# Performance work log

Measured on AMD Instinct MI355X. Metric: run time of the kernel, lower is better.

The kernel has to match this reference:

```python
import jax, jax.numpy as jnp
import numpy as np
import math

N, E, D, G = 100000, 1000000, 64, 128


def setup_inputs() -> dict:
    key = jax.random.key(0)
    ks = jax.random.split(key, 16)
    nrm = lambda k, shape: jax.random.normal(k, shape, jnp.float32) * 0.05
    return {
        "noise_x": jax.random.normal(ks[0], (N, D), jnp.float32),
        "edge_index": jax.random.randint(ks[1], (2, E), 0, N),
        "t": jax.random.randint(ks[2], (1,), 0, 1000),
        "train_anm": jax.random.randint(ks[3], (1000,), 0, N),
        "train_norm": jax.random.randint(ks[4], (5000,), 0, N),
        # time MLP (torch Linear weights stored as [in, out])
        "time_w1": nrm(ks[5], (D, D)), "time_b1": jnp.zeros((D,), jnp.float32),
        "time_w2": nrm(ks[6], (D, D)), "time_b2": jnp.zeros((D,), jnp.float32),
        "label_emb": nrm(ks[7], (2, D)),
        # GCNConv weights: down (D->G, G->G//2), up (G//2->G, 2G->D)
        "w0": nrm(ks[8], (D, G)), "b0": jnp.zeros((G,), jnp.float32),
        "w1": nrm(ks[9], (G, G // 2)), "b1": jnp.zeros((G // 2,), jnp.float32),
        "w2": nrm(ks[10], (G // 2, G)), "b2": jnp.zeros((G,), jnp.float32),
        "w3": nrm(ks[11], (2 * G, D)), "b3": jnp.zeros((D,), jnp.float32),
    }


def silu(x):
    return x * jax.nn.sigmoid(x)


def timestep_embedding(t, dim):
    # standard DDPM sinusoidal embedding; t: [1] int -> [1, dim]
    half = dim // 2
    freqs = jnp.exp(jnp.arange(half, dtype=jnp.float32) * (-math.log(10000.0) / (half - 1)))
    args = t.astype(jnp.float32)[:, None] * freqs[None, :]
    return jnp.concatenate([jnp.sin(args), jnp.cos(args)], axis=1)


def gcn_conv(x, w, b, src, dst, dinv):
    # PyG GCNConv: x' = D^-1/2 (A+I) D^-1/2 (x W) + b
    x = x @ w
    norm = dinv[src] * dinv[dst]                       # [E]
    agg = jax.ops.segment_sum(x[src] * norm[:, None], dst, num_segments=x.shape[0])
    agg = agg + x * (dinv * dinv)[:, None]             # self-loop term
    return agg + b


def reference(noise_x, edge_index, t, train_anm, train_norm,
              time_w1, time_b1, time_w2, time_b2, label_emb,
              w0, b0, w1, b1, w2, b2, w3, b3):
    n, d = noise_x.shape
    src, dst = edge_index[0], edge_index[1]
    # symmetric GCN normalization with self loops: deg = in-degree + 1
    deg = jnp.zeros((n,), jnp.float32).at[dst].add(1.0) + 1.0
    dinv = jax.lax.rsqrt(deg)

    # time embedding MLP (nonlinearity == SiLU)
    temb = timestep_embedding(t, d)
    temb = silu(temb @ time_w1 + time_b1) @ time_w2 + time_b2
    x_t = noise_x + temb                               # broadcast [1,D] over nodes

    # class-conditional label embedding matrix (anm rows set first, then norm)
    lab = jnp.zeros((n, d), noise_x.dtype)
    lab = lab.at[train_anm].set(label_emb[1])
    lab = lab.at[train_norm].set(label_emb[0])
    x_t = x_t + lab

    h0 = silu(gcn_conv(x_t, w0, b0, src, dst, dinv))   # residual link
    h1 = silu(gcn_conv(h0, w1, b1, src, dst, dinv))
    h2 = silu(gcn_conv(h1, w2, b2, src, dst, dinv))
    out = gcn_conv(jnp.concatenate([h2, h0], axis=1), w3, b3, src, dst, dinv)
    return silu(out)
```

## Files before the change

### kernel.cpp

```cpp
#include <hip/hip_runtime.h>
#include <math.h>


typedef unsigned short ushortT;
typedef __attribute__((ext_vector_type(8))) short short8v;
typedef __attribute__((ext_vector_type(4))) float f32x4;

#define CSR_CAP 48

__device__ __forceinline__ ushortT f2bf(float f) {
    unsigned int u = __float_as_uint(f);
    u += 0x7FFFu + ((u >> 16) & 1u);
    return (ushortT)(u >> 16);
}
__device__ __forceinline__ float bf2f(ushortT u) {
    return __uint_as_float(((unsigned int)u) << 16);
}

__global__ __launch_bounds__(256) void prep_kernel(int* __restrict__ cnt,
                                                   int* __restrict__ flag,
                                                   int n, int nblkN, int csBlk,
                                                   int* __restrict__ cs,
                                                   const float* __restrict__ w0,
                                                   const float* __restrict__ w1,
                                                   const float* __restrict__ w2,
                                                   const float* __restrict__ w3,
                                                   ushortT* __restrict__ wdst,
                                                   const int* __restrict__ t,
                                                   const float* __restrict__ tw1,
                                                   const float* __restrict__ tb1,
                                                   const float* __restrict__ tw2,
                                                   const float* __restrict__ tb2,
                                                   float* __restrict__ temb,
                                                   ushortT* __restrict__ bufXT,
                                                   ushortT* __restrict__ xw1) {
    int bid = blockIdx.x;
    if (bid < nblkN) {
        int i = bid * 256 + threadIdx.x;
        if (i < n) { cnt[i] = 0; flag[i] = 0; }
        return;
    }
    if (bid < nblkN + csBlk) {
        size_t total = (size_t)n * CSR_CAP;
        size_t base = ((size_t)(bid - nblkN) * 256 + threadIdx.x) * 16;
        int4 sv = make_int4(n, n, n, n);
#pragma unroll
        for (int j = 0; j < 4; ++j) {
            size_t p = base + j * 4;
            if (p + 4 <= total) *(int4*)(cs + p) = sv;
            else for (size_t q = p; q < total; ++q) cs[q] = n;
        }
        return;
    }
    if (bid < nblkN + csBlk + 160) {
        int i = (bid - nblkN - csBlk) * 256 + threadIdx.x;
        if (i >= 40960) return;
        const float* src; int ST, M, base;
        if (i < 8192)       { src = w0; ST = 8; M = 128; base = 0; }
        else if (i < 16384) { src = w1; ST = 4; M = 64;  base = 8192; }
        else if (i < 24576) { src = w2; ST = 8; M = 128; base = 16384; }
        else                { src = w3; ST = 4; M = 64;  base = 24576; }
        int idx = i - base;
        int j = idx & 7;
        int lane = (idx >> 3) & 63;
        int rest = idx >> 9;
        int s = rest % ST;
        int kq = rest / ST;
        int k = kq * 32 + (lane >> 4) * 8 + j;
        int col = s * 16 + (lane & 15);
        wdst[i] = f2bf(src[(size_t)k * M + col]);
        return;
    }
    __shared__ float emb[64], hid[64];
    int j = threadIdx.x;
    if (j >= 64 && j < 96)  ((unsigned int*)(bufXT + (size_t)n * 64))[j - 64] = 0u;
    if (j >= 96 && j < 128) ((unsigned int*)(xw1 + (size_t)n * 64))[j - 96] = 0u;
    if (j < 64) {
        float tf = (float)t[0];
        int h = j & 31;
        float freq = expf((float)h * -0.29710775393976190f);
        float arg = tf * freq;
        emb[j] = (j < 32) ? sinf(arg) : cosf(arg);
    }
    __syncthreads();
    if (j < 64) {
        float a = tb1[j];
        for (int k = 0; k < 64; ++k) a = fmaf(emb[k], tw1[k * 64 + j], a);
        hid[j] = a / (1.0f + expf(-a));
    }
    __syncthreads();
    if (j < 64) {
        float o = tb2[j];
        for (int k = 0; k < 64; ++k) o = fmaf(hid[k], tw2[k * 64 + j], o);
        temb[j] = o;
    }
}

__global__ __launch_bounds__(256) void flags_kernel(const int* __restrict__ anm, int na,
                                                    const int* __restrict__ nrm, int nn,
                                                    int* __restrict__ flag) {
    int i = blockIdx.x * 256 + threadIdx.x;
    if (i < na) atomicMax(&flag[anm[i]], 1);
    if (i < nn) atomicMax(&flag[nrm[i]], 2);
}

__global__ __launch_bounds__(256) void dinv_kernel(const int* __restrict__ cnt,
                                                   float* __restrict__ dinv, int n) {
    int i = blockIdx.x * 256 + threadIdx.x;
    if (i < n) dinv[i] = rsqrtf((float)cnt[i] + 1.0f);
}

__global__ __launch_bounds__(256) void fill_csr_kernel(const int* __restrict__ ei,
                                                       int* __restrict__ cnt,
                                                       int* __restrict__ cs, int e, int bdiv) {
    int xcd = blockIdx.x & 7;
    int i = (blockIdx.x >> 3) * 256 + threadIdx.x;
    if (i >= e) return;
    int dst = __builtin_nontemporal_load(ei + e + i);
    if (dst / bdiv != xcd) return;
    int src = __builtin_nontemporal_load(ei + i);
    int p = atomicAdd(&cnt[dst], 1);
    if (p < CSR_CAP) cs[(size_t)dst * CSR_CAP + p] = src;
}

__global__ __launch_bounds__(256) void xt_kernel(const float* __restrict__ nx,
                                                 const float* __restrict__ temb,
                                                 const float* __restrict__ lemb,
                                                 const int* __restrict__ flag,
                                                 const float* __restrict__ dinv,
                                                 ushortT* __restrict__ xt, int n) {
    int t = blockIdx.x * 256 + threadIdx.x;
    int total = n * 16;
    if (t >= total) return;
    int row = t >> 4;
    int c4 = (t & 15) * 4;
    float4 v = *(const float4*)(nx + (size_t)row * 64 + c4);
    float4 tv = *(const float4*)(temb + c4);
    v.x += tv.x; v.y += tv.y; v.z += tv.z; v.w += tv.w;
    int f = flag[row];
    if (f) {
        const float* le = lemb + (f == 1 ? 64 : 0);
        float4 lv = *(const float4*)(le + c4);
        v.x += lv.x; v.y += lv.y; v.z += lv.z; v.w += lv.w;
    }
    float dv = dinv[row];
    v.x *= dv; v.y *= dv; v.z *= dv; v.w *= dv;
    unsigned int p0 = (unsigned int)f2bf(v.x) | ((unsigned int)f2bf(v.y) << 16);
    unsigned int p1 = (unsigned int)f2bf(v.z) | ((unsigned int)f2bf(v.w) << 16);
    *(uint2*)(xt + (size_t)row * 64 + c4) = make_uint2(p0, p1);
}

template <int KQT, int ST, bool BIAS_SILU, bool OUT_BF16, bool CAT, bool SCALE>
__global__ __launch_bounds__(256) void mfma_gemm_kernel(const ushortT* __restrict__ A1,
                                                        const ushortT* __restrict__ A2,
                                                        const ushortT* __restrict__ Wswz,
                                                        const float* __restrict__ bias,
                                                        const float* __restrict__ dinvp,
                                                        void* __restrict__ Yv, int n) {
    constexpr int M = ST * 16;
    constexpr int KA = (CAT ? (KQT / 2) : KQT) * 32;
    const int lane = threadIdx.x & 63;
    const int wid = threadIdx.x >> 6;
    const int row0 = blockIdx.x * 64 + wid * 16;
    const int arow = row0 + (lane & 15);
    const int kb = (lane >> 4) * 8;

    f32x4 acc[ST];
#pragma unroll
    for (int s = 0; s < ST; ++s) acc[s] = (f32x4){0.f, 0.f, 0.f, 0.f};

#pragma unroll
    for (int kq = 0; kq < KQT; ++kq) {
        const ushortT* Asrc = (CAT && kq >= KQT / 2) ? A2 : A1;
        const int kloc = (CAT && kq >= KQT / 2) ? (kq - KQT / 2) * 32 : kq * 32;
        short8v a = *(const short8v*)(Asrc + (size_t)arow * KA + kloc + kb);
        const ushortT* wp = Wswz + ((size_t)(kq * ST) * 64 + lane) * 8;
#pragma unroll
        for (int s = 0; s < ST; ++s) {
            short8v b = *(const short8v*)(wp + (size_t)s * 64 * 8);
            acc[s] = __builtin_amdgcn_mfma_f32_16x16x32_bf16(a, b, acc[s], 0, 0, 0);
        }
    }

    const int dcol = lane & 15;
    const int drow0 = row0 + (lane >> 4) * 4;
    float sc[4];
    if (SCALE) {
#pragma unroll
        for (int r = 0; r < 4; ++r) sc[r] = (drow0 + r < n) ? dinvp[drow0 + r] : 0.f;
    }
#pragma unroll
    for (int s = 0; s < ST; ++s) {
        float bv = BIAS_SILU ? bias[s * 16 + dcol] : 0.f;
#pragma unroll
        for (int r = 0; r < 4; ++r) {
            int row = drow0 + r;
            if (row >= n) continue;
            float v = acc[s][r];
            if (BIAS_SILU) { v += bv; v = v / (1.0f + expf(-v)); }
            if (SCALE) v *= sc[r];
            if (OUT_BF16) ((ushortT*)Yv)[(size_t)row * M + s * 16 + dcol] = f2bf(v);
            else          ((float*)Yv)[(size_t)row * M + s * 16 + dcol] = v;
        }
    }
}

template <bool BIAS_SILU, bool OUT_BF16, bool POST_SCALE>
__global__ __launch_bounds__(256) void agg64_kernel(const ushortT* __restrict__ xw,
                                                    const int* __restrict__ cnt,
                                                    const int* __restrict__ cs,
                                                    const float* __restrict__ dinv,
                                                    const float* __restrict__ bias,
                                                    void* __restrict__ yv, int n) {
    int pair = (int)(((size_t)blockIdx.x * 256 + threadIdx.x) >> 6);
    int lane = threadIdx.x & 63;
    int nA = pair * 2;
    int nB = nA + 1;
    if (nA >= n) return;
    bool hasB = (nB < n);
    const int* rA = cs + (size_t)nA * CSR_CAP;
    const int* rB = cs + (size_t)nB * CSR_CAP;

    int ia[16], ib[16];
#pragma unroll
    for (int j = 0; j < 16; ++j) ia[j] = rA[j];
#pragma unroll
    for (int j = 0; j < 16; ++j) ib[j] = hasB ? rB[j] : n;

    float va[16], vb[16];
#pragma unroll
    for (int j = 0; j < 16; ++j) va[j] = bf2f(xw[(size_t)ia[j] * 64 + lane]);
#pragma unroll
    for (int j = 0; j < 16; ++j) vb[j] = bf2f(xw[(size_t)ib[j] * 64 + lane]);

    float a0 = (va[0] + va[1]) + (va[2] + va[3]);
    float a1 = (va[4] + va[5]) + (va[6] + va[7]);
    float a2 = (va[8] + va[9]) + (va[10] + va[11]);
    float a3 = (va[12] + va[13]) + (va[14] + va[15]);
    float b0 = (vb[0] + vb[1]) + (vb[2] + vb[3]);
    float b1 = (vb[4] + vb[5]) + (vb[6] + vb[7]);
    float b2 = (vb[8] + vb[9]) + (vb[10] + vb[11]);
    float b3 = (vb[12] + vb[13]) + (vb[14] + vb[15]);

    int cA = cnt[nA]; if (cA > CSR_CAP) cA = CSR_CAP;
    int cB = hasB ? cnt[nB] : 0; if (cB > CSR_CAP) cB = CSR_CAP;
    for (int j = 16; j < cA; ++j) a0 += bf2f(xw[(size_t)rA[j] * 64 + lane]);
    for (int j = 16; j < cB; ++j) b0 += bf2f(xw[(size_t)rB[j] * 64 + lane]);

    {
        float di = dinv[nA];
        float acc = (a0 + a1) + (a2 + a3);
        acc += bf2f(xw[(size_t)nA * 64 + lane]);
        acc *= di;
        if (BIAS_SILU) {
            acc += bias[lane];
            acc = acc / (1.0f + expf(-acc));
        }
        if (POST_SCALE) acc *= di;
        if (OUT_BF16) ((ushortT*)yv)[(size_t)nA * 64 + lane] = f2bf(acc);
        else          ((float*)yv)[(size_t)nA * 64 + lane] = acc;
    }
    if (hasB) {
        float di = dinv[nB];
        float acc = (b0 + b1) + (b2 + b3);
        acc += bf2f(xw[(size_t)nB * 64 + lane]);
        acc *= di;
        if (BIAS_SILU) {
            acc += bias[lane];
            acc = acc / (1.0f + expf(-acc));
        }
        if (POST_SCALE) acc *= di;
        if (OUT_BF16) ((ushortT*)yv)[(size_t)nB * 64 + lane] = f2bf(acc);
        else          ((float*)yv)[(size_t)nB * 64 + lane] = acc;
    }
}

extern "C" void kernel_launch(void* const* d_in, const int* in_sizes, int n_in,
                              void* d_out, int out_size, void* d_ws, size_t ws_size,
                              hipStream_t stream) {
    const float* noise_x = (const float*)d_in[0];
    const int*   edge    = (const int*)d_in[1];
    const int*   tptr    = (const int*)d_in[2];
    const int*   anm     = (const int*)d_in[3];
    const int*   nrm     = (const int*)d_in[4];
    const float* tw1     = (const float*)d_in[5];
    const float* tb1     = (const float*)d_in[6];
    const float* tw2     = (const float*)d_in[7];
    const float* tb2     = (const float*)d_in[8];
    const float* lemb    = (const float*)d_in[9];
    const float* w0      = (const float*)d_in[10];
    const float* b0      = (const float*)d_in[11];
    const float* w1      = (const float*)d_in[12];
    const float* b1      = (const float*)d_in[13];
    const float* w2      = (const float*)d_in[14];
    const float* b2      = (const float*)d_in[15];
    const float* w3      = (const float*)d_in[16];
    const float* b3      = (const float*)d_in[17];

    const int N = in_sizes[0] / 64;
    const int E = in_sizes[1] / 2;
    const int na = in_sizes[3];
    const int nn = in_sizes[4];
    float* out = (float*)d_out;

    char* ws = (char*)d_ws;
    size_t o = 0;
    auto carve = [&](size_t bytes) -> char* {
        char* p = ws + o;
        o += (bytes + 255) & ~(size_t)255;
        return p;
    };
    int*     cnt      = (int*)carve((size_t)N * 4);
    int*     flag     = (int*)carve((size_t)N * 4);
    int*     cs       = (int*)carve((size_t)N * CSR_CAP * 4);
    float*   dinv     = (float*)carve((size_t)N * 4);
    float*   temb     = (float*)carve(256);
    ushortT* wswz     = (ushortT*)carve(40960 * 2);
    ushortT* bufXT    = (ushortT*)carve((size_t)(N + 1) * 64 * 2);
    ushortT* aggX     = (ushortT*)carve((size_t)N * 64 * 2);
    ushortT* h0       = (ushortT*)carve((size_t)N * 128 * 2);
    ushortT* xw1      = (ushortT*)carve((size_t)(N + 1) * 64 * 2);
    ushortT* aggH1    = (ushortT*)carve((size_t)N * 64 * 2);
    ushortT* h2       = (ushortT*)carve((size_t)N * 128 * 2);
    ushortT* h1s      = bufXT;
    ushortT* z3       = xw1;

    const int nblkN = (N + 255) / 256;
    const int nblkE = (E + 255) / 256;
    const int nmax = na > nn ? na : nn;
    const int aggBlk = (N + 7) / 8;
    const int gblk = (N + 63) / 64;
    const int bdiv = (N + 7) / 8;
    const int csBlk = (int)(((size_t)N * CSR_CAP + 4095) / 4096);

    prep_kernel<<<nblkN + csBlk + 161, 256, 0, stream>>>(cnt, flag, N, nblkN, csBlk, cs,
                                                         w0, w1, w2, w3, wswz,
                                                         tptr, tw1, tb1, tw2, tb2, temb,
                                                         bufXT, xw1);
    flags_kernel<<<(nmax + 255) / 256, 256, 0, stream>>>(anm, na, nrm, nn, flag);
    fill_csr_kernel<<<8 * nblkE, 256, 0, stream>>>(edge, cnt, cs, E, bdiv);
    dinv_kernel<<<nblkN, 256, 0, stream>>>(cnt, dinv, N);
    xt_kernel<<<((size_t)N * 16 + 255) / 256, 256, 0, stream>>>(noise_x, temb, lemb, flag, dinv, bufXT, N);

    agg64_kernel<false, true, false><<<aggBlk, 256, 0, stream>>>(bufXT, cnt, cs, dinv, nullptr, aggX, N);
    mfma_gemm_kernel<2, 8, true, true, false, false><<<gblk, 256, 0, stream>>>(aggX, nullptr, wswz, b0, nullptr, h0, N);
    mfma_gemm_kernel<4, 4, false, true, false, true><<<gblk, 256, 0, stream>>>(h0, nullptr, wswz + 8192, nullptr, dinv, xw1, N);
    agg64_kernel<true, true, true><<<aggBlk, 256, 0, stream>>>(xw1, cnt, cs, dinv, b1, h1s, N);
    agg64_kernel<false, true, false><<<aggBlk, 256, 0, stream>>>(h1s, cnt, cs, dinv, nullptr, aggH1, N);
    mfma_gemm_kernel<2, 8, true, true, false, false><<<gblk, 256, 0, stream>>>(aggH1, nullptr, wswz + 16384, b2, nullptr, h2, N);
    mfma_gemm_kernel<8, 4, false, true, true, true><<<gblk, 256, 0, stream>>>(h2, h0, wswz + 24576, nullptr, dinv, z3, N);
    agg64_kernel<true, false, false><<<aggBlk, 256, 0, stream>>>(z3, cnt, cs, dinv, b3, out, N);
}
```

Measured before the change: 292.3 us.

## Bin edges by destination partition before CSR fill; aggregate four nodes per wave

Replaces the 8x-redundant edge scan (each XCD-targeted block re-reading all edges and filtering) with a two-pass scheme. A binning kernel uses a shared-memory histogram to write (src,dst) pairs into eight destination-range buckets, and a second kernel fills the CSR from each bucket. This cuts repeated reads of the edge list but adds an intermediate pairs buffer write and read. Separately, the aggregation kernel now handles four nodes per wave instead of two, putting more independent gathers in flight at the cost of higher register pressure.

Result: slower. 535.1 us (+83.0%).

```diff
diff --git a/kernel.cpp b/kernel.cpp
--- a/kernel.cpp
+++ b/kernel.cpp
@@ -19,6 +19,7 @@
 
 __global__ __launch_bounds__(256) void prep_kernel(int* __restrict__ cnt,
                                                    int* __restrict__ flag,
+                                                   int* __restrict__ bcnt,
                                                    int n, int nblkN, int csBlk,
                                                    int* __restrict__ cs,
                                                    const float* __restrict__ w0,
@@ -38,6 +39,7 @@
     if (bid < nblkN) {
         int i = bid * 256 + threadIdx.x;
         if (i < n) { cnt[i] = 0; flag[i] = 0; }
+        if (bid == 0 && threadIdx.x < 8) bcnt[threadIdx.x] = 0;
         return;
     }
     if (bid < nblkN + csBlk) {
@@ -110,17 +112,69 @@
     if (i < n) dinv[i] = rsqrtf((float)cnt[i] + 1.0f);
 }
 
-__global__ __launch_bounds__(256) void fill_csr_kernel(const int* __restrict__ ei,
-                                                       int* __restrict__ cnt,
-                                                       int* __restrict__ cs, int e, int bdiv) {
-    int xcd = blockIdx.x & 7;
-    int i = (blockIdx.x >> 3) * 256 + threadIdx.x;
-    if (i >= e) return;
-    int dst = __builtin_nontemporal_load(ei + e + i);
-    if (dst / bdiv != xcd) return;
-    int src = __builtin_nontemporal_load(ei + i);
-    int p = atomicAdd(&cnt[dst], 1);
-    if (p < CSR_CAP) cs[(size_t)dst * CSR_CAP + p] = src;
+__global__ __launch_bounds__(256) void bin_kernel(const int* __restrict__ ei,
+                                                  int* __restrict__ bcnt,
+                                                  int2* __restrict__ pairs,
+                                                  int e, int bdiv, int capb) {
+    __shared__ int hist[8];
+    __shared__ int base[8];
+    __shared__ int cur[8];
+    int t = threadIdx.x;
+    if (t < 8) { hist[t] = 0; cur[t] = 0; }
+    __syncthreads();
+    int i0 = blockIdx.x * 2048 + t;
+    int bk[8], sr[8], ds[8];
+#pragma unroll
+    for (int j = 0; j < 8; ++j) {
+        int i = i0 + j * 256;
+        if (i < e) {
+            ds[j] = __builtin_nontemporal_load(ei + e + i);
+            sr[j] = __builtin_nontemporal_load(ei + i);
+            bk[j] = ds[j] / bdiv;
+            atomicAdd(&hist[bk[j]], 1);
+        } else bk[j] = -1;
+    }
+    __syncthreads();
+    if (t < 8) base[t] = atomicAdd(&bcnt[t], hist[t]);
+    __syncthreads();
+#pragma unroll
+    for (int j = 0; j < 8; ++j) {
+        if (bk[j] >= 0) {
+            int p = atomicAdd(&cur[bk[j]], 1);
+            pairs[(size_t)bk[j] * capb + base[bk[j]] + p] = make_int2(sr[j], ds[j]);
+        }
+    }
+}
+
+__global__ __launch_bounds__(256) void fill_bins_kernel(const int2* __restrict__ pairs,
+                                                        const int* __restrict__ bcnt,
+                                                        int* __restrict__ cnt,
+                                                        int* __restrict__ cs, int capb) {
+    int b = blockIdx.x & 7;
+    int nb = bcnt[b];
+    int tid = (blockIdx.x >> 3) * 256 + threadIdx.x;
+    int stride = (gridDim.x >> 3) * 256;
+    const long long* pll = (const long long*)pairs + (size_t)b * capb;
+    for (int i0 = tid * 4; i0 < nb; i0 += stride * 4) {
+        long long v0 = 0, v1 = 0, v2 = 0, v3 = 0;
+        int m = nb - i0;
+        v0 = __builtin_nontemporal_load(pll + i0);
+        if (m > 1) v1 = __builtin_nontemporal_load(pll + i0 + 1);
+        if (m > 2) v2 = __builtin_nontemporal_load(pll + i0 + 2);
+        if (m > 3) v3 = __builtin_nontemporal_load(pll + i0 + 3);
+        int d0 = (int)(v0 >> 32), s0 = (int)v0;
+        int d1 = (int)(v1 >> 32), s1 = (int)v1;
+        int d2 = (int)(v2 >> 32), s2 = (int)v2;
+        int d3 = (int)(v3 >> 32), s3 = (int)v3;
+        int p0 = atomicAdd(&cnt[d0], 1);
+        int p1 = (m > 1) ? atomicAdd(&cnt[d1], 1) : CSR_CAP;
+        int p2 = (m > 2) ? atomicAdd(&cnt[d2], 1) : CSR_CAP;
+        int p3 = (m > 3) ? atomicAdd(&cnt[d3], 1) : CSR_CAP;
+        if (p0 < CSR_CAP) cs[(size_t)d0 * CSR_CAP + p0] = s0;
+        if (p1 < CSR_CAP) cs[(size_t)d1 * CSR_CAP + p1] = s1;
+        if (p2 < CSR_CAP) cs[(size_t)d2 * CSR_CAP + p2] = s2;
+        if (p3 < CSR_CAP) cs[(size_t)d3 * CSR_CAP + p3] = s3;
+    }
 }
 
 __global__ __launch_bounds__(256) void xt_kernel(const float* __restrict__ nx,
@@ -212,66 +266,61 @@
                                                     const float* __restrict__ dinv,
                                                     const float* __restrict__ bias,
                                                     void* __restrict__ yv, int n) {
-    int pair = (int)(((size_t)blockIdx.x * 256 + threadIdx.x) >> 6);
+    int wv = (int)(((size_t)blockIdx.x * 256 + threadIdx.x) >> 6);
     int lane = threadIdx.x & 63;
-    int nA = pair * 2;
-    int nB = nA + 1;
-    if (nA >= n) return;
-    bool hasB = (nB < n);
-    const int* rA = cs + (size_t)nA * CSR_CAP;
-    const int* rB = cs + (size_t)nB * CSR_CAP;
-
-    int ia[16], ib[16];
-#pragma unroll
-    for (int j = 0; j < 16; ++j) ia[j] = rA[j];
-#pragma unroll
-    for (int j = 0; j < 16; ++j) ib[j] = hasB ? rB[j] : n;
-
-    float va[16], vb[16];
-#pragma unroll
-    for (int j = 0; j < 16; ++j) va[j] = bf2f(xw[(size_t)ia[j] * 64 + lane]);
-#pragma unroll
-    for (int j = 0; j < 16; ++j) vb[j] = bf2f(xw[(size_t)ib[j] * 64 + lane]);
-
-    float a0 = (va[0] + va[1]) + (va[2] + va[3]);
-    float a1 = (va[4] + va[5]) + (va[6] + va[7]);
-    float a2 = (va[8] + va[9]) + (va[10] + va[11]);
-    float a3 = (va[12] + va[13]) + (va[14] + va[15]);
-    float b0 = (vb[0] + vb[1]) + (vb[2] + vb[3]);
-    float b1 = (vb[4] + vb[5]) + (vb[6] + vb[7]);
-    float b2 = (vb[8] + vb[9]) + (vb[10] + vb[11]);
-    float b3 = (vb[12] + vb[13]) + (vb[14] + vb[15]);
-
-    int cA = cnt[nA]; if (cA > CSR_CAP) cA = CSR_CAP;
-    int cB = hasB ? cnt[nB] : 0; if (cB > CSR_CAP) cB = CSR_CAP;
-    for (int j = 16; j < cA; ++j) a0 += bf2f(xw[(size_t)rA[j] * 64 + lane]);
-    for (int j = 16; j < cB; ++j) b0 += bf2f(xw[(size_t)rB[j] * 64 + lane]);
+    int base = wv * 4;
+    if (base >= n) return;
+
+    float accs[4];
+#pragma unroll
+    for (int k = 0; k < 4; ++k) accs[k] = 0.f;
 
     {
-        float di = dinv[nA];
-        float acc = (a0 + a1) + (a2 + a3);
-        acc += bf2f(xw[(size_t)nA * 64 + lane]);
+        float va[4][16];
+#pragma unroll
+        for (int k = 0; k < 4; ++k) {
+            int node = base + k;
+            bool has = (node < n);
+            const int* r = cs + (size_t)(has ? node : 0) * CSR_CAP;
+#pragma unroll
+            for (int j = 0; j < 16; ++j) {
+                int idx = has ? r[j] : n;
+                va[k][j] = bf2f(xw[(size_t)idx * 64 + lane]);
+            }
+        }
+#pragma unroll
+        for (int k = 0; k < 4; ++k) {
+            float s0 = (va[k][0] + va[k][1]) + (va[k][2] + va[k][3]);
+            float s1 = (va[k][4] + va[k][5]) + (va[k][6] + va[k][7]);
+            float s2 = (va[k][8] + va[k][9]) + (va[k][10] + va[k][11]);
+            float s3 = (va[k][12] + va[k][13]) + (va[k][14] + va[k][15]);
+            accs[k] = (s0 + s1) + (s2 + s3);
+        }
+    }
+
+#pragma unroll
+    for (int k = 0; k < 4; ++k) {
+        int node = base + k;
+        if (node >= n) break;
+        int c = cnt[node]; if (c > CSR_CAP) c = CSR_CAP;
+        const int* r = cs + (size_t)node * CSR_CAP;
+        for (int j = 16; j < c; ++j) accs[k] += bf2f(xw[(size_t)r[j] * 64 + lane]);
+    }
+
+#pragma unroll
+    for (int k = 0; k < 4; ++k) {
+        int node = base + k;
+        if (node >= n) break;
+        float di = dinv[node];
+        float acc = accs[k] + bf2f(xw[(size_t)node * 64 + lane]);
         acc *= di;
         if (BIAS_SILU) {
             acc += bias[lane];
             acc = acc / (1.0f + expf(-acc));
         }
         if (POST_SCALE) acc *= di;
-        if (OUT_BF16) ((ushortT*)yv)[(size_t)nA * 64 + lane] = f2bf(acc);
-        else          ((float*)yv)[(size_t)nA * 64 + lane] = acc;
-    }
-    if (hasB) {
-        float di = dinv[nB];
-        float acc = (b0 + b1) + (b2 + b3);
-        acc += bf2f(xw[(size_t)nB * 64 + lane]);
-        acc *= di;
-        if (BIAS_SILU) {
-            acc += bias[lane];
-            acc = acc / (1.0f + expf(-acc));
-        }
-        if (POST_SCALE) acc *= di;
-        if (OUT_BF16) ((ushortT*)yv)[(size_t)nB * 64 + lane] = f2bf(acc);
-        else          ((float*)yv)[(size_t)nB * 64 + lane] = acc;
+        if (OUT_BF16) ((ushortT*)yv)[(size_t)node * 64 + lane] = f2bf(acc);
+        else          ((float*)yv)[(size_t)node * 64 + lane] = acc;
     }
 }
 
@@ -310,8 +359,11 @@
         o += (bytes + 255) & ~(size_t)255;
         return p;
     };
+    const int capb = E / 8 + 8192;
     int*     cnt      = (int*)carve((size_t)N * 4);
     int*     flag     = (int*)carve((size_t)N * 4);
+    int*     bcnt     = (int*)carve(256);
+    int2*    pairs    = (int2*)carve((size_t)capb * 8 * 8);
     int*     cs       = (int*)carve((size_t)N * CSR_CAP * 4);
     float*   dinv     = (float*)carve((size_t)N * 4);
     float*   temb     = (float*)carve(256);
@@ -326,19 +378,20 @@
     ushortT* z3       = xw1;
 
     const int nblkN = (N + 255) / 256;
-    const int nblkE = (E + 255) / 256;
     const int nmax = na > nn ? na : nn;
-    const int aggBlk = (N + 7) / 8;
+    const int aggBlk = (N + 15) / 16;
     const int gblk = (N + 63) / 64;
     const int bdiv = (N + 7) / 8;
+    const int binBlk = (E + 2047) / 2048;
     const int csBlk = (int)(((size_t)N * CSR_CAP + 4095) / 4096);
 
-    prep_kernel<<<nblkN + csBlk + 161, 256, 0, stream>>>(cnt, flag, N, nblkN, csBlk, cs,
+    prep_kernel<<<nblkN + csBlk + 161, 256, 0, stream>>>(cnt, flag, bcnt, N, nblkN, csBlk, cs,
                                                          w0, w1, w2, w3, wswz,
                                                          tptr, tw1, tb1, tw2, tb2, temb,
                                                          bufXT, xw1);
     flags_kernel<<<(nmax + 255) / 256, 256, 0, stream>>>(anm, na, nrm, nn, flag);
-    fill_csr_kernel<<<8 * nblkE, 256, 0, stream>>>(edge, cnt, cs, E, bdiv);
+    bin_kernel<<<binBlk, 256, 0, stream>>>(edge, bcnt, pairs, E, bdiv, capb);
+    fill_bins_kernel<<<8 * 128, 256, 0, stream>>>(pairs, bcnt, cnt, cs, capb);
     dinv_kernel<<<nblkN, 256, 0, stream>>>(cnt, dinv, N);
     xt_kernel<<<((size_t)N * 16 + 255) / 256, 256, 0, stream>>>(noise_x, temb, lemb, flag, dinv, bufXT, N);
 
```
